# Optimization experiments

Measured on AMD Instinct MI355X. Metric: run time of the kernel, lower is better.

The kernel has to match this reference:

```python
import jax, jax.numpy as jnp
import numpy as np
import math

DIM = 512
MIN_THRES = -5.0
MAX_THRES = 7.0


def setup_inputs() -> dict:
    key = jax.random.key(0)
    k1, k2, k3, k4, k5 = jax.random.split(key, 5)
    s_len, batch, dim = 256, 256, DIM
    x = jax.random.normal(k1, (s_len, batch, dim), dtype=jnp.float32)
    # Linear(dim, dim, bias=False) weights, torch convention y = x @ W.T
    Wq = jax.random.normal(k2, (dim, dim), dtype=jnp.float32) * 0.02
    Wk = jax.random.normal(k3, (dim, dim), dtype=jnp.float32) * 0.02
    Wv = jax.random.normal(k4, (dim, dim), dtype=jnp.float32) * 0.02
    root_query = jax.random.normal(k5, (dim,), dtype=jnp.float32)
    return {"x": x, "Wq": Wq, "Wk": Wk, "Wv": Wv, "root_query": root_query}


def _matrix_tree(score):
    # score: [b, s, s]. Batched matrix-tree theorem marginals (lengths=None -> full length).
    b, s, _ = score.shape
    eye = jnp.eye(s, dtype=score.dtype)
    A = jnp.exp(score)                                  # exp(input)
    rd = jnp.exp(jnp.diagonal(score, axis1=1, axis2=2))  # exp(diag) root scores [b, s]
    L_off = A * (1.0 - eye)                              # mask diagonal
    colsum = L_off.sum(axis=1)                           # lap.sum(0): column sums [b, s]
    lap = -L_off + eye * colsum[:, None, :]              # -A_off + diag(colsum)
    lap = lap.at[:, 0, :].set(rd)                        # lap[0] = exp(diag(input))
    inv = jnp.linalg.inv(lap)                            # [b, s, s]
    inv_diag = jnp.diagonal(inv, axis1=1, axis2=2)       # [b, s]
    term1 = A * inv_diag[:, None, :]                     # factor[i,j] = inv_diag[j]
    term2 = A * jnp.swapaxes(inv, 1, 2)
    term1 = term1.at[:, :, 0].set(0.0)
    term2 = term2.at[:, 0, :].set(0.0)
    roots = rd * inv[:, :, 0]                            # diag(input).exp() * inv.T[0]
    return term1 - term2 + roots[:, :, None] * eye       # [b, s, s]


def reference(x, Wq, Wk, Wv, root_query):
    s_len, batch, dim = x.shape
    scale = math.sqrt(1.0 / dim)
    xt = jnp.swapaxes(x, 0, 1)                           # [b, s, d]
    q = jnp.einsum('bsd,ed->bse', xt, Wq)
    k = jnp.einsum('bsd,ed->bse', xt, Wk)
    v = jnp.einsum('bsd,ed->bse', xt, Wv)
    _score = jnp.einsum('bsd,btd->bst', q, k)            # [b, s, s]
    root = jnp.einsum('bsd,d->bs', k, root_query)        # [b, s]
    eye = jnp.eye(s_len, dtype=x.dtype)
    # Faithful to source: score[b] = _score[b]*eye + diag(root[b]) (off-diagonal zeroed)
    score = _score * eye + root[:, :, None] * eye
    score = jnp.clip(score * scale, MIN_THRES, MAX_THRES)
    edge_score = jnp.swapaxes(_matrix_tree(score), 1, 2)  # [b, s, s]
    return jnp.einsum('bst,btd->bsd', edge_score, v)
```

## Files before the change

### kernel.cpp

```cpp
#include <hip/hip_runtime.h>

typedef __bf16 v8bf __attribute__((ext_vector_type(8)));
typedef float f32x4 __attribute__((ext_vector_type(4)));
typedef unsigned short u16x8 __attribute__((ext_vector_type(8)));

#define SLEN 256
#define BATCH 256
#define DIM 512
#define SCALE 0.044194173824159216f

#define TS 64
#define LDX 520
#define LDB 72
#define KC 64

#define MFMA(a, b, c) __builtin_amdgcn_mfma_f32_16x16x32_bf16((a), (b), (c), 0, 0, 0)

__device__ __forceinline__ unsigned int f2bf(float f) {
  union { float f; unsigned int u; } v; v.f = f;
  unsigned int r = v.u + 0x7FFFu + ((v.u >> 16) & 1u);
  return r >> 16;
}
__device__ __forceinline__ float bf2f(unsigned short u) {
  union { unsigned int u; float f; } v; v.u = ((unsigned int)u) << 16;
  return v.f;
}
__device__ __forceinline__ v8bf ld8(const unsigned short* p) {
  u16x8 t = *reinterpret_cast<const u16x8*>(p);
  return __builtin_bit_cast(v8bf, t);
}
__device__ __forceinline__ void gload16(const unsigned short* g, unsigned short* l) {
  __builtin_amdgcn_global_load_lds(
      (const __attribute__((address_space(1))) unsigned int*)g,
      (__attribute__((address_space(3))) unsigned int*)l, 16, 0, 0);
}

__global__ __launch_bounds__(256) void zf(float4* __restrict__ p, int n4) {
  const int i = blockIdx.x * 256 + threadIdx.x;
  if (i < n4) {
    const float4 z = {0.f, 0.f, 0.f, 0.f};
    p[i] = z;
  }
}

__global__ __launch_bounds__(256) void prep_small(const float* __restrict__ Wq,
                                                  const float* __restrict__ Wk,
                                                  const float* __restrict__ Wv,
                                                  const float* __restrict__ rq,
                                                  unsigned short* __restrict__ Mt,
                                                  unsigned short* __restrict__ Wvb,
                                                  float* __restrict__ wkr) {
  __shared__ float As[32][33];
  __shared__ float Bs[32][33];
  const int blk = blockIdx.x;
  const int tid = threadIdx.x;

  if (blk < 256) {
    const int e0 = (blk & 15) * 32;
    const int d0 = (blk >> 4) * 32;
    const int tm = (tid & 15) * 2;
    const int tn = (tid >> 4) * 2;
    const int lf = tid >> 3;
    const int lc = (tid & 7) * 4;
    float a00 = 0.f, a01 = 0.f, a10 = 0.f, a11 = 0.f;
    for (int f0 = 0; f0 < DIM; f0 += 32) {
      __syncthreads();
      const float4 a = *reinterpret_cast<const float4*>(Wk + (size_t)(f0 + lf) * DIM + e0 + lc);
      const float4 b = *reinterpret_cast<const float4*>(Wq + (size_t)(f0 + lf) * DIM + d0 + lc);
      As[lf][lc] = a.x; As[lf][lc + 1] = a.y; As[lf][lc + 2] = a.z; As[lf][lc + 3] = a.w;
      Bs[lf][lc] = b.x; Bs[lf][lc + 1] = b.y; Bs[lf][lc + 2] = b.z; Bs[lf][lc + 3] = b.w;
      __syncthreads();
#pragma unroll
      for (int k = 0; k < 32; ++k) {
        const float x0 = As[k][tm], x1 = As[k][tm + 1];
        const float y0 = Bs[k][tn], y1 = Bs[k][tn + 1];
        a00 += x0 * y0; a01 += x0 * y1; a10 += x1 * y0; a11 += x1 * y1;
      }
    }
    Mt[(size_t)(e0 + tm) * DIM + d0 + tn] = (unsigned short)f2bf(a00);
    Mt[(size_t)(e0 + tm) * DIM + d0 + tn + 1] = (unsigned short)f2bf(a01);
    Mt[(size_t)(e0 + tm + 1) * DIM + d0 + tn] = (unsigned short)f2bf(a10);
    Mt[(size_t)(e0 + tm + 1) * DIM + d0 + tn + 1] = (unsigned short)f2bf(a11);
  } else if (blk < 512) {
    const int idx = ((blk - 256) * 256 + tid) * 4;
    const float4 v = *reinterpret_cast<const float4*>(Wv + idx);
    uint2 p;
    p.x = f2bf(v.x) | (f2bf(v.y) << 16);
    p.y = f2bf(v.z) | (f2bf(v.w) << 16);
    *reinterpret_cast<uint2*>(Wvb + idx) = p;
  } else {
    float* rqs = &As[0][0];
    rqs[tid] = rq[tid];
    rqs[tid + 256] = rq[tid + 256];
    __syncthreads();
    const int d = (blk - 512) * 256 + tid;
    float s = 0.f;
#pragma unroll 8
    for (int f = 0; f < DIM; ++f) s += Wk[(size_t)f * DIM + d] * rqs[f];
    wkr[d] = s;
  }
}

__global__ __launch_bounds__(512, 2) void gemm1_x(const float* __restrict__ X,
                                                  const unsigned short* __restrict__ Mt,
                                                  const float* __restrict__ wkr,
                                                  unsigned short* __restrict__ Xsb,
                                                  float* __restrict__ rdpart) {
  __shared__ unsigned short lds[32768];
  const int tid = threadIdx.x;
  const int lane = tid & 63, w = tid >> 6;
  const int wr = w >> 2, wc = w & 3;
  const int c = lane & 15, g = lane >> 4;
  const int grd = ((g ^ ((c >> 1) & 3))) * 8;

  const int work = (blockIdx.x & 7) * 64 + (blockIdx.x >> 3);
  const int rt = work >> 1, ct = work & 1;
  const int j0 = rt * 256, e0 = ct * 256;

  const int rA = tid >> 1;
  const int h = tid & 1;
  const int sw = (rA >> 1) & 3;
  const int q1 = (2 * h) ^ sw;
  const int q2 = (2 * h + 1) ^ sw;
  const float* xrowp = X + ((size_t)rA * BATCH + rt) * DIM;
  unsigned short* xsrow = Xsb + ((size_t)rA * BATCH + rt) * DIM;

  const int rB = tid >> 2;
  const int glB = (tid & 3) ^ ((rB >> 1) & 3);
  const unsigned short* sBp = Mt + (size_t)(e0 + rB) * DIM + glB * 8;

#define LOADA1(t, va, vb, vc, vd) {                                             \
    const int kc_ = (t) * 32;                                                   \
    va = *reinterpret_cast<const float4*>(xrowp + kc_ + q1 * 8);                \
    vb = *reinterpret_cast<const float4*>(xrowp + kc_ + q1 * 8 + 4);            \
    vc = *reinterpret_cast<const float4*>(xrowp + kc_ + q2 * 8);                \
    vd = *reinterpret_cast<const float4*>(xrowp + kc_ + q2 * 8 + 4); }

#define WRITEA1(t, va, vb, vc, vd) {                                            \
    const int kc_ = (t) * 32;                                                   \
    unsigned short* lb_ = lds + ((t) & 1) * 16384;                              \
    uint4 p1, p2;                                                               \
    p1.x = f2bf(va.x) | (f2bf(va.y) << 16);                                     \
    p1.y = f2bf(va.z) | (f2bf(va.w) << 16);                                     \
    p1.z = f2bf(vb.x) | (f2bf(vb.y) << 16);                                     \
    p1.w = f2bf(vb.z) | (f2bf(vb.w) << 16);                                     \
    p2.x = f2bf(vc.x) | (f2bf(vc.y) << 16);                                     \
    p2.y = f2bf(vc.z) | (f2bf(vc.w) << 16);                                     \
    p2.z = f2bf(vd.x) | (f2bf(vd.y) << 16);                                     \
    p2.w = f2bf(vd.z) | (f2bf(vd.w) << 16);                                     \
    *reinterpret_cast<uint4*>(lb_ + rA * 32 + (2 * h) * 8) = p1;                \
    *reinterpret_cast<uint4*>(lb_ + rA * 32 + (2 * h + 1) * 8) = p2;            \
    if (((t) >> 3) == ct) {               \
      *reinterpret_cast<uint4*>(xsrow + kc_ + q1 * 8) = p1;                     \
      *reinterpret_cast<uint4*>(xsrow + kc_ + q2 * 8) = p2;                     \
    } }

#define GLOADB1(t) {                                                            \
    const int kc_ = (t) * 32;                                                   \
    unsigned short* lb_ = lds + ((t) & 1) * 16384 + 8192 + (w << 9);            \
    gload16(sBp + kc_, lb_);                                                    \
    gload16(sBp + kc_ + (size_t)128 * DIM, lb_ + 4096); }

  f32x4 acc[8][4] = {};
  {
    float4 a0, a1, a2, a3;
    LOADA1(0, a0, a1, a2, a3);
    GLOADB1(0);
    WRITEA1(0, a0, a1, a2, a3);
  }
  __syncthreads();
  for (int t = 0; t < 16; ++t) {
    const int cur = t & 1;
    float4 n0, n1, n2, n3;
    if (t < 15) {
      LOADA1(t + 1, n0, n1, n2, n3);
      GLOADB1(t + 1);
    }
    const unsigned short* la = lds + cur * 16384;
    const unsigned short* lb2 = la + 8192;
    v8bf a[8], bbf[4];
#pragma unroll
    for (int m = 0; m < 8; ++m) a[m] = ld8(la + (wr * 128 + m * 16 + c) * 32 + grd);
#pragma unroll
    for (int n = 0; n < 4; ++n) bbf[n] = ld8(lb2 + (wc * 64 + n * 16 + c) * 32 + grd);
    __builtin_amdgcn_s_setprio(1);
#pragma unroll
    for (int m = 0; m < 8; ++m)
#pragma unroll
      for (int n = 0; n < 4; ++n) acc[m][n] = MFMA(a[m], bbf[n], acc[m][n]);
    __builtin_amdgcn_s_setprio(0);
    if (t < 15) WRITEA1(t + 1, n0, n1, n2, n3);
    __syncthreads();
  }

  float* red = (float*)lds;
  float wkrl[4];
#pragma unroll
  for (int n = 0; n < 4; ++n) wkrl[n] = wkr[e0 + wc * 64 + n * 16 + c];
#pragma unroll
  for (int m = 0; m < 8; ++m) {
#pragma unroll
    for (int i = 0; i < 4; ++i) {
      const int rl = wr * 128 + m * 16 + 4 * g + i;
      const unsigned short* xrow = Xsb + ((size_t)rl * BATCH + rt) * DIM + e0 + wc * 64 + c;
      float val = 0.f;
#pragma unroll
      for (int n = 0; n < 4; ++n)
        val += (acc[m][n][i] + wkrl[n]) * bf2f(xrow[n * 16]);
      val += __shfl_xor(val, 1); val += __shfl_xor(val, 2);
      val += __shfl_xor(val, 4); val += __shfl_xor(val, 8);
      if (c == 0) red[wc * 256 + rl] = val;
    }
  }
  __syncthreads();
  if (tid < 256) {
    const float s = red[tid] + red[256 + tid] + red[512 + tid] + red[768 + tid];
    rdpart[(size_t)ct * 65536 + j0 + tid] = s;
  }
}

#define GEMM_PROLOGUE()                                                         \
  f32x4 acc[8][4] = {};                                                         \
  STG(0); STG(1); STG(2);

#define GEMM_MAIN_LOOP()                                                        \
  for (int t = 0; t < 16; ++t) {                                                \
    if (t <= 13) { asm volatile("s_waitcnt vmcnt(8)" ::: "memory"); }           \
    else if (t == 14) { asm volatile("s_waitcnt vmcnt(4)" ::: "memory"); }      \
    else { asm volatile("s_waitcnt vmcnt(0)" ::: "memory"); }                   \
    __builtin_amdgcn_s_barrier();                                               \
    __builtin_amdgcn_sched_barrier(0);                                          \
    if (t + 3 < 16) { STG(t + 3); }                                             \
    __builtin_amdgcn_sched_barrier(0);                                          \
    const unsigned short* la = ldsp + (t & 3) * 16384;                          \
    const unsigned short* lb2 = la + 8192;                                      \
    v8bf a[8], bbf[4];                                                          \
    _Pragma("unroll")                                                           \
    for (int m = 0; m < 8; ++m)                                                 \
      a[m] = ld8(la + (wr * 128 + m * 16 + c) * 32 + grd);                      \
    _Pragma("unroll")                                                           \
    for (int n = 0; n < 4; ++n)                                                 \
      bbf[n] = ld8(lb2 + (wc * 64 + n * 16 + c) * 32 + grd);                    \
    __builtin_amdgcn_s_setprio(1);                                              \
    _Pragma("unroll")                                                           \
    for (int m = 0; m < 8; ++m)                                                 \
      _Pragma("unroll")                                                         \
      for (int n = 0; n < 4; ++n) acc[m][n] = MFMA(a[m], bbf[n], acc[m][n]);    \
    __builtin_amdgcn_s_setprio(0);                                              \
  }

#define STG(tt) {                                                               \
    const int kc_ = (tt) * 32;                                                  \
    unsigned short* lb_ = lw + ((tt) & 3) * 16384;                              \
    gload16(sAp + kc_, lb_);                                                    \
    gload16(sAp + kc_ + sA2, lb_ + 4096);                                       \
    gload16(sBp + kc_, lb_ + 8192);                                             \
    gload16(sBp + kc_ + sB2, lb_ + 12288); }

__global__ __launch_bounds__(512, 2) void gemm2_f(const unsigned short* __restrict__ Xsb,
                                                  const unsigned short* __restrict__ Wvb,
                                                  const float* __restrict__ rdpart,
                                                  float* __restrict__ out) {
  __shared__ unsigned short ldsp[65536];
  __shared__ float rdl[256];
  __shared__ float wsum[4];
  const int tid = threadIdx.x;
  const int lane = tid & 63, w = tid >> 6;
  const int wr = w >> 2, wc = w & 3;
  const int c = lane & 15, g = lane >> 4;
  const int grd = ((g ^ ((c >> 1) & 3))) * 8;

  const int work = (blockIdx.x & 7) * 64 + (blockIdx.x >> 3);
  const int rt = work >> 1, ct = work & 1;
  const int j0 = rt * 256, e0 = ct * 256;
  const int b = rt;

  if (tid < 256) {
    float v = (rdpart[(size_t)b * SLEN + tid] + rdpart[65536 + (size_t)b * SLEN + tid]) * SCALE;
    v = fminf(fmaxf(v, -5.0f), 7.0f);
    const float r = expf(v);
    rdl[tid] = r;
    float t = r;
    t += __shfl_xor(t, 1);  t += __shfl_xor(t, 2);  t += __shfl_xor(t, 4);
    t += __shfl_xor(t, 8);  t += __shfl_xor(t, 16); t += __shfl_xor(t, 32);
    if ((tid & 63) == 0) wsum[tid >> 6] = t;
  }
  __syncthreads();

  const int rA = tid >> 2;
  const int gl = (tid & 3) ^ ((rA >> 1) & 3);
  const unsigned short* sAp = Xsb + ((size_t)rA * BATCH + b) * DIM + gl * 8;
  const unsigned short* sBp = Wvb + (size_t)rA * DIM + gl * 8;
  const size_t sA2 = (size_t)128 * BATCH * DIM;
  const size_t sB2 = (size_t)128 * DIM;
  unsigned short* lw = ldsp + (w << 9);
  const unsigned short* sBp2 = sBp + (size_t)e0 * DIM;
  sBp = sBp2;

  GEMM_PROLOGUE()
  GEMM_MAIN_LOOP()

  float vsp[4] = {0.f, 0.f, 0.f, 0.f}, vwp[4] = {0.f, 0.f, 0.f, 0.f};
#pragma unroll
  for (int m = 0; m < 8; ++m) {
#pragma unroll
    for (int i = 0; i < 4; ++i) {
      const int rl = wr * 128 + m * 16 + 4 * g + i;
      const float rr = rdl[rl];
#pragma unroll
      for (int n = 0; n < 4; ++n) {
        vsp[n] += acc[m][n][i];
        vwp[n] += rr * acc[m][n][i];
      }
    }
  }
#pragma unroll
  for (int n = 0; n < 4; ++n) {
    vsp[n] += __shfl_xor(vsp[n], 16); vsp[n] += __shfl_xor(vsp[n], 32);
    vwp[n] += __shfl_xor(vwp[n], 16); vwp[n] += __shfl_xor(vwp[n], 32);
  }
  __syncthreads();
  float* red = (float*)ldsp;
  if (g == 0) {
#pragma unroll
    for (int n = 0; n < 4; ++n) {
      red[(w * 4 + n) * 16 + c] = vsp[n];
      red[512 + (w * 4 + n) * 16 + c] = vwp[n];
    }
  }
  __syncthreads();
  const float Rb = wsum[0] + wsum[1] + wsum[2] + wsum[3];
  const float invR = 1.0f / Rb;
  const float gam = invR * 0.00390625f;
  const int wo = w ^ 4;
  float vsf[4], vwf[4];
#pragma unroll
  for (int n = 0; n < 4; ++n) {
    vsf[n] = red[(w * 4 + n) * 16 + c] + red[(wo * 4 + n) * 16 + c];
    vwf[n] = red[512 + (w * 4 + n) * 16 + c] + red[512 + (wo * 4 + n) * 16 + c];
  }
#pragma unroll
  for (int m = 0; m < 8; ++m) {
#pragma unroll
    for (int i = 0; i < 4; ++i) {
      const int rl = wr * 128 + m * 16 + 4 * g + i;
      const float tt = rdl[rl] * invR;
      const float al = tt - 0.00390625f;
      const float be = (1.0f - tt) * 0.00390625f;
      float* orow = out + (size_t)(j0 + rl) * DIM + e0 + wc * 64 + c;
#pragma unroll
      for (int n = 0; n < 4; ++n)
        orow[n * 16] = al * acc[m][n][i] + be * vsf[n] + gam * vwf[n];
    }
  }
}

__global__ __launch_bounds__(256) void prep_mt(const float* __restrict__ Wq,
                                               const float* __restrict__ Wk,
                                               unsigned short* __restrict__ Mt) {
  __shared__ float As[32][33];
  __shared__ float Bs[32][33];
  const int e0 = (blockIdx.x & 15) * 32;
  const int d0 = (blockIdx.x >> 4) * 32;
  const int tid = threadIdx.x;
  const int tm = (tid & 15) * 2;
  const int tn = (tid >> 4) * 2;
  const int lf = tid >> 3;
  const int lc = (tid & 7) * 4;
  float a00 = 0.f, a01 = 0.f, a10 = 0.f, a11 = 0.f;
  for (int f0 = 0; f0 < DIM; f0 += 32) {
    __syncthreads();
    const float4 a = *reinterpret_cast<const float4*>(Wk + (size_t)(f0 + lf) * DIM + e0 + lc);
    const float4 b = *reinterpret_cast<const float4*>(Wq + (size_t)(f0 + lf) * DIM + d0 + lc);
    As[lf][lc] = a.x; As[lf][lc + 1] = a.y; As[lf][lc + 2] = a.z; As[lf][lc + 3] = a.w;
    Bs[lf][lc] = b.x; Bs[lf][lc + 1] = b.y; Bs[lf][lc + 2] = b.z; Bs[lf][lc + 3] = b.w;
    __syncthreads();
#pragma unroll
    for (int k = 0; k < 32; ++k) {
      const float x0 = As[k][tm], x1 = As[k][tm + 1];
      const float y0 = Bs[k][tn], y1 = Bs[k][tn + 1];
      a00 += x0 * y0; a01 += x0 * y1; a10 += x1 * y0; a11 += x1 * y1;
    }
  }
  Mt[(size_t)(e0 + tm) * DIM + d0 + tn] = (unsigned short)f2bf(a00);
  Mt[(size_t)(e0 + tm) * DIM + d0 + tn + 1] = (unsigned short)f2bf(a01);
  Mt[(size_t)(e0 + tm + 1) * DIM + d0 + tn] = (unsigned short)f2bf(a10);
  Mt[(size_t)(e0 + tm + 1) * DIM + d0 + tn + 1] = (unsigned short)f2bf(a11);
}

__global__ __launch_bounds__(256) void conv_wv(const float* __restrict__ Wv,
                                               unsigned short* __restrict__ Wvb) {
  const int idx = (blockIdx.x * 256 + threadIdx.x) * 4;
  const float4 v = *reinterpret_cast<const float4*>(Wv + idx);
  uint2 p;
  p.x = f2bf(v.x) | (f2bf(v.y) << 16);
  p.y = f2bf(v.z) | (f2bf(v.w) << 16);
  *reinterpret_cast<uint2*>(Wvb + idx) = p;
}

__global__ __launch_bounds__(256) void wkr_k2(const float* __restrict__ Wk,
                                              const float* __restrict__ rq,
                                              float* __restrict__ wkr) {
  __shared__ float rqs[DIM];
  const int tid = threadIdx.x;
  rqs[tid] = rq[tid];
  rqs[tid + 256] = rq[tid + 256];
  __syncthreads();
  const int d = blockIdx.x * 256 + tid;
  float s = 0.f;
#pragma unroll 8
  for (int f = 0; f < DIM; ++f) s += Wk[(size_t)f * DIM + d] * rqs[f];
  wkr[d] = s;
}

__global__ __launch_bounds__(256, 2) void pass1_fb(
    const float* __restrict__ X, const unsigned short* __restrict__ Mt,
    const float* __restrict__ wkr, float* __restrict__ rd_out,
    float* __restrict__ Rsum, float* __restrict__ xsum, float* __restrict__ xw) {
  __shared__ __align__(16) unsigned short Xs[TS * LDX];
  __shared__ __align__(16) unsigned short Bsh[64 * LDB];
  __shared__ float wkrs[DIM];
  __shared__ float dacc[TS];
  __shared__ float rds[TS];
  const int tid = threadIdx.x;
  const int b = blockIdx.x & 255;
  const int s0 = (blockIdx.x >> 8) * TS;
  const int lane = tid & 63;
  const int wave = tid >> 6;
  const int wr = wave >> 1, wc = wave & 1;
  const int g = lane >> 4, c = lane & 15;
#pragma unroll 4
  for (int r = 0; r < TS; ++r) {
    const float2 v = *reinterpret_cast<const float2*>(
        X + ((size_t)(s0 + r) * BATCH + b) * DIM + tid * 2);
    Xs[r * LDX + tid * 2] = (unsigned short)f2bf(v.x);
    Xs[r * LDX + tid * 2 + 1] = (unsigned short)f2bf(v.y);
  }
  wkrs[tid] = wkr[tid];
  wkrs[tid + 256] = wkr[tid + 256];
  if (tid < TS) dacc[tid] = 0.f;
  float dp0[4] = {0.f, 0.f, 0.f, 0.f};
  float dp1[4] = {0.f, 0.f, 0.f, 0.f};
  for (int et = 0; et < 8; ++et) {
    const int e0 = et * 64;
    f32x4 acc00 = {0.f,0.f,0.f,0.f}, acc01 = {0.f,0.f,0.f,0.f};
    f32x4 acc10 = {0.f,0.f,0.f,0.f}, acc11 = {0.f,0.f,0.f,0.f};
    for (int kc0 = 0; kc0 < DIM; kc0 += KC) {
      __syncthreads();
      {
        const int e = tid >> 2;
        const int kq = (tid & 3) * 16;
        const uint4* src = reinterpret_cast<const uint4*>(Mt + (size_t)(e0 + e) * DIM + kc0 + kq);
        const uint4 w0 = src[0];
        const uint4 w1 = src[1];
        *reinterpret_cast<uint4*>(&Bsh[e * LDB + kq]) = w0;
        *reinterpret_cast<uint4*>(&Bsh[e * LDB + kq + 8]) = w1;
      }
      __syncthreads();
#pragma unroll
      for (int ks = 0; ks < KC; ks += 32) {
        const int ka = kc0 + ks + 8 * g;
        const int kb = ks + 8 * g;
        const v8bf fa0 = ld8(&Xs[(32 * wr + c) * LDX + ka]);
        const v8bf fa1 = ld8(&Xs[(32 * wr + 16 + c) * LDX + ka]);
        const v8bf fb0 = ld8(&Bsh[(32 * wc + c) * LDB + kb]);
        const v8bf fb1 = ld8(&Bsh[(32 * wc + 16 + c) * LDB + kb]);
        acc00 = MFMA(fa0, fb0, acc00);
        acc01 = MFMA(fa0, fb1, acc01);
        acc10 = MFMA(fa1, fb0, acc10);
        acc11 = MFMA(fa1, fb1, acc11);
      }
    }
#pragma unroll
    for (int i = 0; i < 4; ++i) {
      const int r0 = 32 * wr + 4 * g + i;
      const int ec0 = e0 + 32 * wc + c;
      const float w0 = wkrs[ec0], w1 = wkrs[ec0 + 16];
      dp0[i] += (acc00[i] + w0) * bf2f(Xs[r0 * LDX + ec0]) +
                (acc01[i] + w1) * bf2f(Xs[r0 * LDX + ec0 + 16]);
      dp1[i] += (acc10[i] + w0) * bf2f(Xs[(r0 + 16) * LDX + ec0]) +
                (acc11[i] + w1) * bf2f(Xs[(r0 + 16) * LDX + ec0 + 16]);
    }
  }
#pragma unroll
  for (int i = 0; i < 4; ++i) {
    float v0 = dp0[i], v1 = dp1[i];
    v0 += __shfl_xor(v0, 1); v0 += __shfl_xor(v0, 2);
    v0 += __shfl_xor(v0, 4); v0 += __shfl_xor(v0, 8);
    v1 += __shfl_xor(v1, 1); v1 += __shfl_xor(v1, 2);
    v1 += __shfl_xor(v1, 4); v1 += __shfl_xor(v1, 8);
    if (c == 0) {
      atomicAdd(&dacc[32 * wr + 4 * g + i], v0);
      atomicAdd(&dacc[32 * wr + 16 + 4 * g + i], v1);
    }
  }
  __syncthreads();
  if (tid < TS) {
    float sc = dacc[tid] * SCALE;
    sc = fminf(fmaxf(sc, -5.0f), 7.0f);
    const float r = expf(sc);
    rds[tid] = r;
    rd_out[(size_t)b * SLEN + s0 + tid] = r;
    float t = r;
    t += __shfl_xor(t, 1); t += __shfl_xor(t, 2); t += __shfl_xor(t, 4);
    t += __shfl_xor(t, 8); t += __shfl_xor(t, 16); t += __shfl_xor(t, 32);
    if (tid == 0) atomicAdd(&Rsum[b], t);
  }
  __syncthreads();
#pragma unroll
  for (int dd = 0; dd < 2; ++dd) {
    const int d = tid + dd * 256;
    float s1 = 0.f, s2 = 0.f;
    for (int r = 0; r < TS; ++r) {
      const float xv = bf2f(Xs[r * LDX + d]);
      s1 += xv;
      s2 += rds[r] * xv;
    }
    atomicAdd(&xsum[(size_t)b * DIM + d], s1);
    atomicAdd(&xw[(size_t)b * DIM + d], s2);
  }
}

__global__ __launch_bounds__(256, 2) void pass2_fb(
    const float* __restrict__ X, const unsigned short* __restrict__ Wvb,
    const float* __restrict__ rd, const float* __restrict__ Rsum,
    const float* __restrict__ xsum, const float* __restrict__ xw,
    float* __restrict__ out) {
  __shared__ __align__(16) unsigned short Zs[TS * LDX];
  __shared__ __align__(16) unsigned short Bsh[64 * LDB];
  __shared__ float xss[DIM];
  __shared__ float xws[DIM];
  __shared__ float rds[TS];
  const int tid = threadIdx.x;
  const int b = blockIdx.x & 255;
  const int s0 = (blockIdx.x >> 8) * TS;
  const int lane = tid & 63;
  const int wave = tid >> 6;
  const int wr = wave >> 1, wc = wave & 1;
  const int g = lane >> 4, c = lane & 15;
  xss[tid] = xsum[(size_t)b * DIM + tid];
  xss[tid + 256] = xsum[(size_t)b * DIM + tid + 256];
  xws[tid] = xw[(size_t)b * DIM + tid];
  xws[tid + 256] = xw[(size_t)b * DIM + tid + 256];
  if (tid < TS) rds[tid] = rd[(size_t)b * SLEN + s0 + tid];
  const float Rb = Rsum[b];
  const float invR = 1.0f / Rb;
  const float gam = invR * (1.0f / 256.0f);
  __syncthreads();
#pragma unroll 4
  for (int r = 0; r < TS; ++r) {
    const float rv = rds[r];
    const float al = rv * invR - (1.0f / 256.0f);
    const float be = (1.0f - rv * invR) * (1.0f / 256.0f);
    const float2 v = *reinterpret_cast<const float2*>(
        X + ((size_t)(s0 + r) * BATCH + b) * DIM + tid * 2);
    const int d0 = tid * 2;
    Zs[r * LDX + d0] = (unsigned short)f2bf(al * v.x + be * xss[d0] + gam * xws[d0]);
    Zs[r * LDX + d0 + 1] = (unsigned short)f2bf(al * v.y + be * xss[d0 + 1] + gam * xws[d0 + 1]);
  }
  const size_t outbase = ((size_t)b * SLEN + s0) * DIM;
  for (int et = 0; et < 8; ++et) {
    const int e0 = et * 64;
    f32x4 acc00 = {0.f,0.f,0.f,0.f}, acc01 = {0.f,0.f,0.f,0.f};
    f32x4 acc10 = {0.f,0.f,0.f,0.f}, acc11 = {0.f,0.f,0.f,0.f};
    for (int kc0 = 0; kc0 < DIM; kc0 += KC) {
      __syncthreads();
      {
        const int e = tid >> 2;
        const int kq = (tid & 3) * 16;
        const uint4* src = reinterpret_cast<const uint4*>(Wvb + (size_t)(e0 + e) * DIM + kc0 + kq);
        const uint4 w0 = src[0];
        const uint4 w1 = src[1];
        *reinterpret_cast<uint4*>(&Bsh[e * LDB + kq]) = w0;
        *reinterpret_cast<uint4*>(&Bsh[e * LDB + kq + 8]) = w1;
      }
      __syncthreads();
#pragma unroll
      for (int ks = 0; ks < KC; ks += 32) {
        const int ka = kc0 + ks + 8 * g;
        const int kb = ks + 8 * g;
        const v8bf fa0 = ld8(&Zs[(32 * wr + c) * LDX + ka]);
        const v8bf fa1 = ld8(&Zs[(32 * wr + 16 + c) * LDX + ka]);
        const v8bf fb0 = ld8(&Bsh[(32 * wc + c) * LDB + kb]);
        const v8bf fb1 = ld8(&Bsh[(32 * wc + 16 + c) * LDB + kb]);
        acc00 = MFMA(fa0, fb0, acc00);
        acc01 = MFMA(fa0, fb1, acc01);
        acc10 = MFMA(fa1, fb0, acc10);
        acc11 = MFMA(fa1, fb1, acc11);
      }
    }
#pragma unroll
    for (int i = 0; i < 4; ++i) {
      const int r0 = 32 * wr + 4 * g + i;
      const int c0 = e0 + 32 * wc + c;
      out[outbase + (size_t)r0 * DIM + c0] = acc00[i];
      out[outbase + (size_t)r0 * DIM + c0 + 16] = acc01[i];
      out[outbase + (size_t)(r0 + 16) * DIM + c0] = acc10[i];
      out[outbase + (size_t)(r0 + 16) * DIM + c0 + 16] = acc11[i];
    }
  }
}

extern "C" void kernel_launch(void* const* d_in, const int* in_sizes, int n_in,
                              void* d_out, int out_size, void* d_ws, size_t ws_size,
                              hipStream_t stream) {
  (void)in_sizes; (void)n_in; (void)out_size;
  const float* X = (const float*)d_in[0];
  const float* Wq = (const float*)d_in[1];
  const float* Wk = (const float*)d_in[2];
  const float* Wv = (const float*)d_in[3];
  const float* rq = (const float*)d_in[4];
  float* out = (float*)d_out;
  char* ws = (char*)d_ws;

  unsigned short* Mt = (unsigned short*)(ws + 0);
  unsigned short* Wvb = (unsigned short*)(ws + 524288);

  const size_t NEED = 69206016;
  if (ws_size >= NEED) {
    float* wkr = (float*)(ws + 1048576);
    float* rdpart = (float*)(ws + 1052672);
    unsigned short* Xsb = (unsigned short*)(ws + 2097152);

    prep_small<<<dim3(514), dim3(256), 0, stream>>>(Wq, Wk, Wv, rq, Mt, Wvb, wkr);
    gemm1_x<<<dim3(512), dim3(512), 0, stream>>>(X, Mt, wkr, Xsb, rdpart);
    gemm2_f<<<dim3(512), dim3(512), 0, stream>>>(Xsb, Wvb, rdpart, out);
  } else {
    float* rd = (float*)(ws + 1048576);
    float* wkr = (float*)(ws + 1310720);
    float* Rsum = (float*)(ws + 1312768);
    float* xsum = (float*)(ws + 1313792);
    float* xw = (float*)(ws + 1838080);
    zf<<<dim3(257), dim3(256), 0, stream>>>((float4*)(ws + 1310720), 65728);
    prep_mt<<<dim3(256), dim3(256), 0, stream>>>(Wq, Wk, Mt);
    conv_wv<<<dim3(256), dim3(256), 0, stream>>>(Wv, Wvb);
    wkr_k2<<<dim3(2), dim3(256), 0, stream>>>(Wk, rq, wkr);
    pass1_fb<<<dim3(1024), dim3(256), 0, stream>>>(X, Mt, wkr, rd, Rsum, xsum, xw);
    pass2_fb<<<dim3(1024), dim3(256), 0, stream>>>(X, Wvb, rd, Rsum, xsum, xw, out);
  }
}
```

Measured before the change: 187.4 us.

## Deepen A-load prefetch to two stages with explicit vmcnt waits in first GEMM

The first GEMM loop now loads the fp32 X rows two k-steps ahead into alternating register sets, while the B tile is still loaded one step ahead. Explicit s_waitcnt vmcnt values, sched_barriers and a raw s_barrier replace __syncthreads, so global loads stay in flight across the MFMA block. The aim is to hide global-load latency behind compute, at the cost of more registers, which may lower occupancy. The hand-counted vmcnt values are fragile and must match the exact number of outstanding loads. A small pointer-arithmetic cleanup for Wvb is also included.

```diff
diff --git a/kernel.cpp b/kernel.cpp
--- a/kernel.cpp
+++ b/kernel.cpp
@@ -129,69 +129,120 @@
   const int glB = (tid & 3) ^ ((rB >> 1) & 3);
   const unsigned short* sBp = Mt + (size_t)(e0 + rB) * DIM + glB * 8;
 
-#define LOADA1(t, va, vb, vc, vd) {                                             \
-    const int kc_ = (t) * 32;                                                   \
-    va = *reinterpret_cast<const float4*>(xrowp + kc_ + q1 * 8);                \
-    vb = *reinterpret_cast<const float4*>(xrowp + kc_ + q1 * 8 + 4);            \
-    vc = *reinterpret_cast<const float4*>(xrowp + kc_ + q2 * 8);                \
-    vd = *reinterpret_cast<const float4*>(xrowp + kc_ + q2 * 8 + 4); }
-
-#define WRITEA1(t, va, vb, vc, vd) {                                            \
-    const int kc_ = (t) * 32;                                                   \
-    unsigned short* lb_ = lds + ((t) & 1) * 16384;                              \
-    uint4 p1, p2;                                                               \
-    p1.x = f2bf(va.x) | (f2bf(va.y) << 16);                                     \
-    p1.y = f2bf(va.z) | (f2bf(va.w) << 16);                                     \
-    p1.z = f2bf(vb.x) | (f2bf(vb.y) << 16);                                     \
-    p1.w = f2bf(vb.z) | (f2bf(vb.w) << 16);                                     \
-    p2.x = f2bf(vc.x) | (f2bf(vc.y) << 16);                                     \
-    p2.y = f2bf(vc.z) | (f2bf(vc.w) << 16);                                     \
-    p2.z = f2bf(vd.x) | (f2bf(vd.y) << 16);                                     \
-    p2.w = f2bf(vd.z) | (f2bf(vd.w) << 16);                                     \
-    *reinterpret_cast<uint4*>(lb_ + rA * 32 + (2 * h) * 8) = p1;                \
-    *reinterpret_cast<uint4*>(lb_ + rA * 32 + (2 * h + 1) * 8) = p2;            \
-    if (((t) >> 3) == ct) {               \
-      *reinterpret_cast<uint4*>(xsrow + kc_ + q1 * 8) = p1;                     \
-      *reinterpret_cast<uint4*>(xsrow + kc_ + q2 * 8) = p2;                     \
-    } }
-
-#define GLOADB1(t) {                                                            \
+#define GB1(t) {                                                                \
     const int kc_ = (t) * 32;                                                   \
     unsigned short* lb_ = lds + ((t) & 1) * 16384 + 8192 + (w << 9);            \
     gload16(sBp + kc_, lb_);                                                    \
     gload16(sBp + kc_ + (size_t)128 * DIM, lb_ + 4096); }
 
+#define LA2(t, A0, A1, A2, A3) {                                                \
+    const int kc_ = (t) * 32;                                                   \
+    A0 = *reinterpret_cast<const float4*>(xrowp + kc_ + q1 * 8);                \
+    A1 = *reinterpret_cast<const float4*>(xrowp + kc_ + q1 * 8 + 4);            \
+    A2 = *reinterpret_cast<const float4*>(xrowp + kc_ + q2 * 8);                \
+    A3 = *reinterpret_cast<const float4*>(xrowp + kc_ + q2 * 8 + 4); }
+
+#define PW1(t, A0, A1, A2, A3) {                                                \
+    unsigned short* lb_ = lds + ((t) & 1) * 16384;                              \
+    uint4 p1, p2;                                                               \
+    p1.x = f2bf(A0.x) | (f2bf(A0.y) << 16);                                     \
+    p1.y = f2bf(A0.z) | (f2bf(A0.w) << 16);                                     \
+    p1.z = f2bf(A1.x) | (f2bf(A1.y) << 16);                                     \
+    p1.w = f2bf(A1.z) | (f2bf(A1.w) << 16);                                     \
+    p2.x = f2bf(A2.x) | (f2bf(A2.y) << 16);                                     \
+    p2.y = f2bf(A2.z) | (f2bf(A2.w) << 16);                                     \
+    p2.z = f2bf(A3.x) | (f2bf(A3.y) << 16);                                     \
+    p2.w = f2bf(A3.z) | (f2bf(A3.w) << 16);                                     \
+    *reinterpret_cast<uint4*>(lb_ + rA * 32 + (2 * h) * 8) = p1;                \
+    *reinterpret_cast<uint4*>(lb_ + rA * 32 + (2 * h + 1) * 8) = p2; }
+
+#define SX1(t, A0, A1, A2, A3) {                                                \
+    const int kc_ = (t) * 32;                                                   \
+    uint4 p1, p2;                                                               \
+    p1.x = f2bf(A0.x) | (f2bf(A0.y) << 16);                                     \
+    p1.y = f2bf(A0.z) | (f2bf(A0.w) << 16);                                     \
+    p1.z = f2bf(A1.x) | (f2bf(A1.y) << 16);                                     \
+    p1.w = f2bf(A1.z) | (f2bf(A1.w) << 16);                                     \
+    p2.x = f2bf(A2.x) | (f2bf(A2.y) << 16);                                     \
+    p2.y = f2bf(A2.z) | (f2bf(A2.w) << 16);                                     \
+    p2.z = f2bf(A3.x) | (f2bf(A3.y) << 16);                                     \
+    p2.w = f2bf(A3.z) | (f2bf(A3.w) << 16);                                     \
+    *reinterpret_cast<uint4*>(xsrow + kc_ + q1 * 8) = p1;                       \
+    *reinterpret_cast<uint4*>(xsrow + kc_ + q2 * 8) = p2; }
+
+#define CMP1(t) {                                                               \
+    const unsigned short* la = lds + ((t) & 1) * 16384;                         \
+    const unsigned short* lb2 = la + 8192;                                      \
+    v8bf a[8], bbf[4];                                                          \
+    _Pragma("unroll")                                                           \
+    for (int m = 0; m < 8; ++m)                                                 \
+      a[m] = ld8(la + (wr * 128 + m * 16 + c) * 32 + grd);                      \
+    _Pragma("unroll")                                                           \
+    for (int n = 0; n < 4; ++n)                                                 \
+      bbf[n] = ld8(lb2 + (wc * 64 + n * 16 + c) * 32 + grd);                    \
+    __builtin_amdgcn_s_setprio(1);                                              \
+    _Pragma("unroll")                                                           \
+    for (int m = 0; m < 8; ++m)                                                 \
+      _Pragma("unroll")                                                         \
+      for (int n = 0; n < 4; ++n) acc[m][n] = MFMA(a[m], bbf[n], acc[m][n]);    \
+    __builtin_amdgcn_s_setprio(0); }
+
+#define SUBITER(T, L0, L1, L2, L3, W0, W1, W2, W3)                              \
+  {                                                                             \
+    const int t_ = (T);                                                         \
+    if (t_ + 1 < 16) { GB1(t_ + 1); }                                           \
+    __builtin_amdgcn_sched_barrier(0);                                          \
+    if (t_ + 2 < 16) { LA2(t_ + 2, L0, L1, L2, L3); }                           \
+    __builtin_amdgcn_sched_barrier(0);                                          \
+    CMP1(t_);                                                                   \
+    if (t_ + 1 < 16) {                                                          \
+      if (t_ <= 13) {                                                           \
+        if ((t_ >> 3) == ct) { asm volatile("s_waitcnt vmcnt(8)" ::: "memory"); }\
+        else                 { asm volatile("s_waitcnt vmcnt(6)" ::: "memory"); }\
+      } else {                                                                  \
+        if (ct == 1) { asm volatile("s_waitcnt vmcnt(4)" ::: "memory"); }       \
+        else         { asm volatile("s_waitcnt vmcnt(2)" ::: "memory"); }       \
+      }                                                                         \
+      __builtin_amdgcn_sched_barrier(0);                                        \
+      PW1(t_ + 1, W0, W1, W2, W3);                                              \
+      if (t_ <= 13) { asm volatile("s_waitcnt vmcnt(4)" ::: "memory"); }        \
+      else          { asm volatile("s_waitcnt vmcnt(0)" ::: "memory"); }        \
+      __builtin_amdgcn_sched_barrier(0);                                        \
+      if (((t_ + 1) >> 3) == ct) { SX1(t_ + 1, W0, W1, W2, W3); }               \
+      asm volatile("s_waitcnt lgkmcnt(0)" ::: "memory");                        \
+      __builtin_amdgcn_sched_barrier(0);                                        \
+      __builtin_amdgcn_s_barrier();                                             \
+    }                                                                           \
+  }
+
   f32x4 acc[8][4] = {};
-  {
-    float4 a0, a1, a2, a3;
-    LOADA1(0, a0, a1, a2, a3);
-    GLOADB1(0);
-    WRITEA1(0, a0, a1, a2, a3);
-  }
-  __syncthreads();
-  for (int t = 0; t < 16; ++t) {
-    const int cur = t & 1;
-    float4 n0, n1, n2, n3;
-    if (t < 15) {
-      LOADA1(t + 1, n0, n1, n2, n3);
-      GLOADB1(t + 1);
-    }
-    const unsigned short* la = lds + cur * 16384;
-    const unsigned short* lb2 = la + 8192;
-    v8bf a[8], bbf[4];
-#pragma unroll
-    for (int m = 0; m < 8; ++m) a[m] = ld8(la + (wr * 128 + m * 16 + c) * 32 + grd);
-#pragma unroll
-    for (int n = 0; n < 4; ++n) bbf[n] = ld8(lb2 + (wc * 64 + n * 16 + c) * 32 + grd);
-    __builtin_amdgcn_s_setprio(1);
-#pragma unroll
-    for (int m = 0; m < 8; ++m)
-#pragma unroll
-      for (int n = 0; n < 4; ++n) acc[m][n] = MFMA(a[m], bbf[n], acc[m][n]);
-    __builtin_amdgcn_s_setprio(0);
-    if (t < 15) WRITEA1(t + 1, n0, n1, n2, n3);
-    __syncthreads();
-  }
+  float4 ea0, ea1, ea2, ea3, oa0, oa1, oa2, oa3;
+
+  GB1(0);
+  __builtin_amdgcn_sched_barrier(0);
+  LA2(0, ea0, ea1, ea2, ea3);
+  LA2(1, oa0, oa1, oa2, oa3);
+  __builtin_amdgcn_sched_barrier(0);
+  asm volatile("s_waitcnt vmcnt(4)" ::: "memory");
+  __builtin_amdgcn_sched_barrier(0);
+  PW1(0, ea0, ea1, ea2, ea3);
+  if (ct == 0) { SX1(0, ea0, ea1, ea2, ea3); }
+  asm volatile("s_waitcnt lgkmcnt(0)" ::: "memory");
+  __builtin_amdgcn_sched_barrier(0);
+  __builtin_amdgcn_s_barrier();
+
+  for (int tt = 0; tt < 16; tt += 2) {
+    SUBITER(tt,     ea0, ea1, ea2, ea3, oa0, oa1, oa2, oa3);
+    SUBITER(tt + 1, oa0, oa1, oa2, oa3, ea0, ea1, ea2, ea3);
+  }
+  __syncthreads();
+
+#undef GB1
+#undef LA2
+#undef PW1
+#undef SX1
+#undef CMP1
+#undef SUBITER
 
   float* red = (float*)lds;
   float wkrl[4];
@@ -290,12 +341,10 @@
   const int rA = tid >> 2;
   const int gl = (tid & 3) ^ ((rA >> 1) & 3);
   const unsigned short* sAp = Xsb + ((size_t)rA * BATCH + b) * DIM + gl * 8;
-  const unsigned short* sBp = Wvb + (size_t)rA * DIM + gl * 8;
+  const unsigned short* sBp = Wvb + (size_t)(e0 + rA) * DIM + gl * 8;
   const size_t sA2 = (size_t)128 * BATCH * DIM;
   const size_t sB2 = (size_t)128 * DIM;
   unsigned short* lw = ldsp + (w << 9);
-  const unsigned short* sBp2 = sBp + (size_t)e0 * DIM;
-  sBp = sBp2;
 
   GEMM_PROLOGUE()
   GEMM_MAIN_LOOP()
```

New measurement: 191.9 us. 2.4% more time.
